# Kernel tuning notes

Hardware: AMD Instinct MI355X
Metric: run time of the kernel (lower is better)

## Reference

```python
import jax, jax.numpy as jnp
import numpy as np

N = 100000   # nodes
E = 1600000  # edges
G = 64       # graphs
D = 64       # latent_dim
NF = 128     # num_node_feats
EF = 32      # num_edge_feats
NV = 5000    # num_node_val_feats
LV = 3       # max_lv
EPS = 1e-5


def setup_inputs() -> dict:
    key = jax.random.key(0)
    ks = jax.random.split(key, 16)
    s = 0.05
    return {
        "node_feat": jax.random.normal(ks[0], (N, NF), jnp.float32),
        "edge_feat": jax.random.normal(ks[1], (E, EF), jnp.float32),
        "w_n2l_W": jax.random.normal(ks[2], (NF, D), jnp.float32) * s,
        "w_n2l_b": jnp.zeros((D,), jnp.float32),
        "node_val_embedding": jax.random.normal(ks[3], (NV, D), jnp.float32) * s,
        "w_e2l_W": jax.random.normal(ks[4], (LV + 1, EF, D), jnp.float32) * s,
        "w_e2l_b": jnp.zeros((LV + 1, D), jnp.float32),
        "conv_W": jax.random.normal(ks[5], (LV, D, D), jnp.float32) * s,
        "conv_b": jnp.zeros((LV, D), jnp.float32),
        "l2_W": jax.random.normal(ks[6], (LV, D, D), jnp.float32) * s,
        "l2_b": jnp.zeros((LV, D), jnp.float32),
        "msg_g": jnp.ones((LV + 1, D), jnp.float32),
        "msg_b": jnp.zeros((LV + 1, D), jnp.float32),
        "hid_g": jnp.ones((LV, D), jnp.float32),
        "hid_b": jnp.zeros((LV, D), jnp.float32),
        "out_W": jax.random.normal(ks[7], (D, D), jnp.float32) * s,
        "out_b": jnp.zeros((D,), jnp.float32),
        "edge_from": jax.random.randint(ks[8], (E,), 0, N, jnp.int32),
        "edge_to": jax.random.randint(ks[9], (E,), 0, N, jnp.int32),
        "g_idx": jnp.sort(jax.random.randint(ks[10], (N,), 0, G, jnp.int32)),
        "node_val_idx": jax.random.randint(ks[11], (N,), 0, NV, jnp.int32),
    }


def _bn(x, g, b):
    # BatchNorm1d in training mode: biased batch stats
    m = jnp.mean(x, axis=0)
    v = jnp.mean(jnp.square(x - m), axis=0)
    return (x - m) * jax.lax.rsqrt(v + EPS) * g + b


def reference(node_feat, edge_feat, w_n2l_W, w_n2l_b, node_val_embedding,
              w_e2l_W, w_e2l_b, conv_W, conv_b, l2_W, l2_b,
              msg_g, msg_b, hid_g, hid_b, out_W, out_b,
              edge_from, edge_to, g_idx, node_val_idx):
    act = jax.nn.relu
    # input node transform + sparse node-value embedding (one-hot spmm == gather)
    h = node_feat @ w_n2l_W + w_n2l_b + node_val_embedding[node_val_idx]
    # edge->node pool for level 0
    e0 = edge_feat @ w_e2l_W[0] + w_e2l_b[0]
    h = h + jax.ops.segment_sum(e0, edge_to, num_segments=N)
    h = _bn(act(h), msg_g[0], msg_b[0])
    for lv in range(LV):
        # MessagePassing with add-aggr: gather sources, scatter-add to targets, then Linear
        agg = jax.ops.segment_sum(h[edge_from], edge_to, num_segments=N)
        node_linear = agg @ conv_W[lv] + conv_b[lv]
        e = edge_feat @ w_e2l_W[lv + 1] + w_e2l_b[lv + 1]
        merged = act(node_linear + jax.ops.segment_sum(e, edge_to, num_segments=N))
        merged = _bn(merged, hid_g[lv], hid_b[lv])
        h = _bn(act(merged @ l2_W[lv] + l2_b[lv] + h), msg_g[lv + 1], msg_b[lv + 1])
    # readout: gnn_out='last', readout_agg='max', act_last=True, bn=False
    pooled = jax.ops.segment_max(h, g_idx, num_segments=G)
    return act(pooled @ out_W + out_b)
```

## Files before the change

kernel.cpp:

```cpp
#include <hip/hip_runtime.h>
#include <math.h>

#define NN 100000
#define EE 1600000
#define GG 64
#define DD 64
#define NF 128
#define EF 32
#define LVL 3
#define EPSBN 1e-5f
#define NTILES ((NN + 63) / 64)
#define NBKT 391

typedef unsigned short u16;
typedef unsigned int u32;
typedef short s4v __attribute__((ext_vector_type(4)));
typedef short bf16x8 __attribute__((ext_vector_type(8)));
typedef float f32x4 __attribute__((ext_vector_type(4)));

__device__ __forceinline__ float4 ld4(const float* p) { return *(const float4*)p; }
__device__ __forceinline__ u16 f2b(float f) {
    u32 u = __float_as_uint(f);
    return (u16)((u + 0x7FFFu + ((u >> 16) & 1u)) >> 16);
}
__device__ __forceinline__ float b2f(u16 u) { return __uint_as_float(((u32)u) << 16); }
__device__ __forceinline__ float blo(u32 u) { return __uint_as_float(u << 16); }
__device__ __forceinline__ float bhi(u32 u) { return __uint_as_float(u & 0xFFFF0000u); }


__global__ void k1b(const int* __restrict__ to, int* __restrict__ bhist) {
    __shared__ int h[NBKT];
    for (int i = threadIdx.x; i < NBKT; i += 256) h[i] = 0;
    __syncthreads();
    for (int e = blockIdx.x * 256 + threadIdx.x; e < EE; e += 256 * gridDim.x)
        atomicAdd(&h[to[e] >> 8], 1);
    __syncthreads();
    for (int i = threadIdx.x; i < NBKT; i += 256)
        if (h[i]) atomicAdd(&bhist[i], h[i]);
}

__global__ void k1c(const int* __restrict__ bhist, int* __restrict__ bbase,
                    int* __restrict__ gcur) {
    __shared__ int s[512];
    int t = threadIdx.x;
    s[t] = (t < NBKT) ? bhist[t] : 0;
    __syncthreads();
    for (int off = 1; off < 512; off <<= 1) {
        int v = (t >= off) ? s[t - off] : 0;
        __syncthreads();
        s[t] += v;
        __syncthreads();
    }
    if (t < NBKT) {
        int base = t ? s[t - 1] : 0;
        bbase[t] = base;
        gcur[t] = base;
    }
    if (t == NBKT - 1) bbase[NBKT] = s[t];
}

__global__ void k1d(const int* __restrict__ to, const int* __restrict__ from,
                    int* __restrict__ gcur, int2* __restrict__ tmp) {
    __shared__ int h[NBKT];
    __shared__ int cur[NBKT];
    for (int i = threadIdx.x; i < NBKT; i += 256) h[i] = 0;
    __syncthreads();
    for (int e = blockIdx.x * 256 + threadIdx.x; e < EE; e += 256 * gridDim.x)
        atomicAdd(&h[to[e] >> 8], 1);
    __syncthreads();
    for (int i = threadIdx.x; i < NBKT; i += 256)
        cur[i] = h[i] ? atomicAdd(&gcur[i], h[i]) : 0;
    __syncthreads();
    for (int e = blockIdx.x * 256 + threadIdx.x; e < EE; e += 256 * gridDim.x) {
        int tt = to[e];
        int b = tt >> 8;
        int pos = atomicAdd(&cur[b], 1);
        tmp[pos] = make_int2(from[e] | ((tt & 255) << 17), e);
    }
}

__global__ void kp2(const int2* __restrict__ tmp, const int* __restrict__ bbase,
                    int* __restrict__ row_ptr, int2* __restrict__ pair) {
    __shared__ int s[256];
    __shared__ int cur[256];
    int b = blockIdx.x, t = threadIdx.x;
    int e0 = bbase[b], e1 = bbase[b + 1];
    s[t] = 0;
    __syncthreads();
    for (int e = e0 + t; e < e1; e += 256) atomicAdd(&s[(tmp[e].x >> 17) & 255], 1);
    __syncthreads();
    int v = s[t];
    for (int off = 1; off < 256; off <<= 1) {
        int u = (t >= off) ? s[t - off] : 0;
        __syncthreads();
        s[t] += u;
        __syncthreads();
    }
    int excl = e0 + s[t] - v;
    cur[t] = excl;
    int n = b * 256 + t;
    if (n < NN) row_ptr[n] = excl;
    if (b == NBKT - 1 && t == 0) row_ptr[NN] = e1;
    __syncthreads();
    for (int e = e0 + t; e < e1; e += 256) {
        int2 w = tmp[e];
        int pos = atomicAdd(&cur[(w.x >> 17) & 255], 1);
        pair[pos] = make_int2(w.y, w.x & 0x1FFFF);
    }
}

__global__ void kpool(const float* __restrict__ ef, const int* __restrict__ row_ptr,
                      const int2* __restrict__ pair, u16* __restrict__ pooled) {
    int lane = threadIdx.x & 63;
    int wid = threadIdx.x >> 6;
    int w = lane & 31, half = lane >> 5;
    for (int n = blockIdx.x * 4 + wid; n < NN; n += gridDim.x * 4) {
        int e0 = row_ptr[n], e1 = row_ptr[n + 1];
        float acc = 0.f;
        int e = e0 + half;
        for (; e + 6 < e1; e += 8) {
            int i0 = pair[e].x, i1 = pair[e + 2].x;
            int i2 = pair[e + 4].x, i3 = pair[e + 6].x;
            float v0 = ef[(size_t)i0 * EF + w];
            float v1 = ef[(size_t)i1 * EF + w];
            float v2 = ef[(size_t)i2 * EF + w];
            float v3 = ef[(size_t)i3 * EF + w];
            acc += (v0 + v1) + (v2 + v3);
        }
        for (; e < e1; e += 2) acc += ef[(size_t)pair[e].x * EF + w];
        acc += __shfl_xor(acc, 32);
        if (half == 0) pooled[(size_t)n * EF + w] = f2b(acc);
    }
}

template <int K1, int K2, bool A1BF, bool AAFF, bool EMB, bool BE, bool RESID>
__global__ __launch_bounds__(256) void kgemm_mfma(
    const void* __restrict__ A1v, const u16* __restrict__ A2,
    const float* __restrict__ W1, const float* __restrict__ W2,
    const float* __restrict__ bias, const float* __restrict__ be,
    const int* __restrict__ row_ptr, const float* __restrict__ emb,
    const int* __restrict__ nvi, const u16* __restrict__ resid,
    const float* __restrict__ raff, const float* __restrict__ aaff,
    u16* __restrict__ Xb, float* __restrict__ stats) {
    constexpr int K = K1 + K2;
    constexpr int KP = K + 8;
    __shared__ u16 A_lds[64 * KP];
    __shared__ u16 Wt_lds[64 * KP];
    __shared__ float red[128];

    const int t = threadIdx.x;
    const int lane = t & 63;
    const int wv = t >> 6;
    const int l15 = lane & 15;
    const int lg = lane >> 4;

    for (int idx = t; idx < K * 16; idx += 256) {
        int k = idx >> 4, c4 = (idx & 15) * 4;
        float4 w4 = (k < K1) ? ld4(W1 + (size_t)k * 64 + c4)
                             : ld4(W2 + (size_t)(k - K1) * 64 + c4);
        Wt_lds[(c4 + 0) * KP + k] = f2b(w4.x);
        Wt_lds[(c4 + 1) * KP + k] = f2b(w4.y);
        Wt_lds[(c4 + 2) * KP + k] = f2b(w4.z);
        Wt_lds[(c4 + 3) * KP + k] = f2b(w4.w);
    }
    if (t < 128) red[t] = 0.f;

    float bias_c[4], be_c[4], rsc_c[4], rsh_c[4];
#pragma unroll
    for (int n = 0; n < 4; n++) {
        int ch = 16 * n + l15;
        bias_c[n] = bias[ch];
        be_c[n] = BE ? be[ch] : 0.f;
        rsc_c[n] = RESID ? raff[ch] : 0.f;
        rsh_c[n] = RESID ? raff[64 + ch] : 0.f;
    }

    for (int tile = blockIdx.x; tile < NTILES; tile += gridDim.x) {
        int nb = tile * 64;
        __syncthreads();
        if (A1BF) {
            const u16* A1b = (const u16*)A1v;
            for (int idx = t; idx < 64 * (K1 / 4); idx += 256) {
                int node = idx / (K1 / 4), kq = (idx % (K1 / 4)) * 4;
                int gn = nb + node;
                s4v v = {0, 0, 0, 0};
                if (gn < NN) {
                    v = *(const s4v*)(A1b + (size_t)gn * K1 + kq);
                    if (AAFF) {
#pragma unroll
                        for (int i = 0; i < 4; i++) {
                            float f = b2f((u16)v[i]) * aaff[kq + i] + aaff[64 + kq + i];
                            v[i] = (short)f2b(f);
                        }
                    }
                }
                *(s4v*)&A_lds[node * KP + kq] = v;
            }
        } else {
            const float* A1f = (const float*)A1v;
            for (int idx = t; idx < 64 * (K1 / 4); idx += 256) {
                int node = idx / (K1 / 4), kq = (idx % (K1 / 4)) * 4;
                int gn = nb + node;
                s4v v = {0, 0, 0, 0};
                if (gn < NN) {
                    float4 a = ld4(A1f + (size_t)gn * K1 + kq);
                    v[0] = (short)f2b(a.x); v[1] = (short)f2b(a.y);
                    v[2] = (short)f2b(a.z); v[3] = (short)f2b(a.w);
                }
                *(s4v*)&A_lds[node * KP + kq] = v;
            }
        }
        if (K2 > 0) {
            for (int idx = t; idx < 64 * (K2 / 4); idx += 256) {
                int node = idx / (K2 / 4), kq = (idx % (K2 / 4)) * 4;
                int gn = nb + node;
                s4v v = {0, 0, 0, 0};
                if (gn < NN) v = *(const s4v*)(A2 + (size_t)gn * K2 + kq);
                *(s4v*)&A_lds[node * KP + K1 + kq] = v;
            }
        }
        __syncthreads();

        f32x4 acc[4];
#pragma unroll
        for (int n = 0; n < 4; n++) acc[n] = (f32x4){0.f, 0.f, 0.f, 0.f};
        const int arow = 16 * wv + l15;
#pragma unroll
        for (int kk = 0; kk < K; kk += 32) {
            s4v alo = *(const s4v*)&A_lds[arow * KP + kk + lg * 4];
            s4v ahi = *(const s4v*)&A_lds[arow * KP + kk + lg * 4 + 16];
            bf16x8 a = __builtin_shufflevector(alo, ahi, 0, 1, 2, 3, 4, 5, 6, 7);
#pragma unroll
            for (int n = 0; n < 4; n++) {
                s4v wlo = *(const s4v*)&Wt_lds[(16 * n + l15) * KP + kk + lg * 4];
                s4v whi = *(const s4v*)&Wt_lds[(16 * n + l15) * KP + kk + lg * 4 + 16];
                bf16x8 b = __builtin_shufflevector(wlo, whi, 0, 1, 2, 3, 4, 5, 6, 7);
                acc[n] = __builtin_amdgcn_mfma_f32_16x16x32_bf16(a, b, acc[n], 0, 0, 0);
            }
        }

        float ss[4] = {0, 0, 0, 0}, sq2[4] = {0, 0, 0, 0};
#pragma unroll
        for (int r = 0; r < 4; r++) {
            int node = nb + 16 * wv + lg * 4 + r;
            if (node < NN) {
                float deg = BE ? (float)(row_ptr[node + 1] - row_ptr[node]) : 0.f;
                int nv = EMB ? nvi[node] : 0;
#pragma unroll
                for (int n = 0; n < 4; n++) {
                    int ch = 16 * n + l15;
                    float v = acc[n][r] + bias_c[n];
                    if (BE) v += deg * be_c[n];
                    if (EMB) v += emb[(size_t)nv * 64 + ch];
                    if (RESID) v += b2f(resid[(size_t)node * 64 + ch]) * rsc_c[n] + rsh_c[n];
                    v = fmaxf(v, 0.f);
                    Xb[(size_t)node * 64 + ch] = f2b(v);
                    ss[n] += v;
                    sq2[n] += v * v;
                }
            }
        }
#pragma unroll
        for (int n = 0; n < 4; n++) {
            float a = ss[n];
            a += __shfl_xor(a, 16);
            a += __shfl_xor(a, 32);
            float b = sq2[n];
            b += __shfl_xor(b, 16);
            b += __shfl_xor(b, 32);
            if (lg == 0) {
                atomicAdd(&red[16 * n + l15], a);
                atomicAdd(&red[64 + 16 * n + l15], b);
            }
        }
    }
    __syncthreads();
    if (t < 128) atomicAdd(&stats[t], red[t]);
}

__global__ void kfin(float* __restrict__ stats, const float* __restrict__ g,
                     const float* __restrict__ b, int slot) {
    int t = threadIdx.x;
    float mean = stats[t] * (1.0f / NN);
    float var = stats[64 + t] * (1.0f / NN) - mean * mean;
    float rstd = rsqrtf(fmaxf(var, 0.f) + EPSBN);
    float sc = g[t] * rstd;
    float* slotp = stats + 128 + slot * 128;
    slotp[t] = sc;
    slotp[64 + t] = b[t] - mean * sc;
    stats[t] = 0.f;
    stats[64 + t] = 0.f;
}

__global__ void kmsg_bf(const u32* __restrict__ h2, const int* __restrict__ row_ptr,
                        const int2* __restrict__ pair, const float* __restrict__ aff,
                        u32* __restrict__ agg) {
    int lane = threadIdx.x & 63;
    int wid = threadIdx.x >> 6;
    int w = lane & 31, half = lane >> 5;
    float sc0 = aff[2 * w], sc1 = aff[2 * w + 1];
    float sh0 = aff[64 + 2 * w], sh1 = aff[64 + 2 * w + 1];
    for (int n = blockIdx.x * 4 + wid; n < NN; n += gridDim.x * 4) {
        int e0 = row_ptr[n], e1 = row_ptr[n + 1];
        float a0 = 0.f, a1 = 0.f;
        int e = e0;
        for (; e + 16 <= e1; e += 16) {
            int s0 = pair[e + half].y, s1 = pair[e + 2 + half].y;
            int s2 = pair[e + 4 + half].y, s3 = pair[e + 6 + half].y;
            int s4 = pair[e + 8 + half].y, s5 = pair[e + 10 + half].y;
            int s6 = pair[e + 12 + half].y, s7 = pair[e + 14 + half].y;
            u32 u0 = h2[(size_t)s0 * 32 + w];
            u32 u1 = h2[(size_t)s1 * 32 + w];
            u32 u2 = h2[(size_t)s2 * 32 + w];
            u32 u3 = h2[(size_t)s3 * 32 + w];
            u32 u4 = h2[(size_t)s4 * 32 + w];
            u32 u5 = h2[(size_t)s5 * 32 + w];
            u32 u6 = h2[(size_t)s6 * 32 + w];
            u32 u7 = h2[(size_t)s7 * 32 + w];
            a0 += ((blo(u0) + blo(u1)) + (blo(u2) + blo(u3))) +
                  ((blo(u4) + blo(u5)) + (blo(u6) + blo(u7)));
            a1 += ((bhi(u0) + bhi(u1)) + (bhi(u2) + bhi(u3))) +
                  ((bhi(u4) + bhi(u5)) + (bhi(u6) + bhi(u7)));
        }
        for (; e + 8 <= e1; e += 8) {
            int s0 = pair[e + half].y, s1 = pair[e + 2 + half].y;
            int s2 = pair[e + 4 + half].y, s3 = pair[e + 6 + half].y;
            u32 u0 = h2[(size_t)s0 * 32 + w];
            u32 u1 = h2[(size_t)s1 * 32 + w];
            u32 u2 = h2[(size_t)s2 * 32 + w];
            u32 u3 = h2[(size_t)s3 * 32 + w];
            a0 += (blo(u0) + blo(u1)) + (blo(u2) + blo(u3));
            a1 += (bhi(u0) + bhi(u1)) + (bhi(u2) + bhi(u3));
        }
        for (; e < e1; e += 2) {
            if (e + half < e1) {
                u32 u = h2[(size_t)pair[e + half].y * 32 + w];
                a0 += blo(u);
                a1 += bhi(u);
            }
        }
        a0 += __shfl_xor(a0, 32);
        a1 += __shfl_xor(a1, 32);
        if (half == 0) {
            float deg = (float)(e1 - e0);
            u16 o0 = f2b(sc0 * a0 + deg * sh0);
            u16 o1 = f2b(sc1 * a1 + deg * sh1);
            agg[(size_t)n * 32 + w] = (u32)o0 | ((u32)o1 << 16);
        }
    }
}

__device__ __forceinline__ unsigned fenc(float f) {
    unsigned u = __float_as_uint(f);
    return (u >> 31) ? ~u : (u | 0x80000000u);
}
__device__ __forceinline__ float fdec(unsigned k) {
    return (k >> 31) ? __uint_as_float(k ^ 0x80000000u) : __uint_as_float(~k);
}

__global__ void kinitpk(unsigned* __restrict__ pk) {
    int i = blockIdx.x * blockDim.x + threadIdx.x;
    if (i < GG * DD) pk[i] = 0x007FFFFFu;
}

__global__ void kread(const u16* __restrict__ h2, const int* __restrict__ gidx,
                      const float* __restrict__ aff, unsigned* __restrict__ pk) {
    int lane = threadIdx.x & 63;
    int wid = threadIdx.x >> 6;
    float sc = aff[lane], sh = aff[64 + lane];
    int gw = blockIdx.x * 4 + wid;
    int nw = gridDim.x * 4;
    int chunk = (NN + nw - 1) / nw;
    int lo = gw * chunk, hi = min(lo + chunk, NN);
    if (lo >= hi) return;
    int cur = gidx[lo];
    float acc = -INFINITY;
    for (int n = lo; n < hi; n++) {
        int g = gidx[n];
        if (g != cur) {
            atomicMax(&pk[cur * DD + lane], fenc(acc));
            cur = g;
            acc = -INFINITY;
        }
        acc = fmaxf(acc, b2f(h2[(size_t)n * 64 + lane]) * sc + sh);
    }
    atomicMax(&pk[cur * DD + lane], fenc(acc));
}

__global__ void kout(const unsigned* __restrict__ pk, const float* __restrict__ W,
                     const float* __restrict__ b, float* __restrict__ out) {
    int t = blockIdx.x * blockDim.x + threadIdx.x;
    int g = t >> 6, d = t & 63;
    float acc = b[d];
    for (int k = 0; k < DD; k++) {
        float p = fdec(pk[g * DD + k]);
        acc += p * W[k * DD + d];
    }
    out[t] = fmaxf(acc, 0.f);
}

extern "C" void kernel_launch(void* const* d_in, const int* in_sizes, int n_in,
                              void* d_out, int out_size, void* d_ws, size_t ws_size,
                              hipStream_t stream) {
    const float* node_feat = (const float*)d_in[0];
    const float* edge_feat = (const float*)d_in[1];
    const float* w_n2l_W = (const float*)d_in[2];
    const float* w_n2l_b = (const float*)d_in[3];
    const float* nve = (const float*)d_in[4];
    const float* w_e2l_W = (const float*)d_in[5];
    const float* w_e2l_b = (const float*)d_in[6];
    const float* conv_W = (const float*)d_in[7];
    const float* conv_b = (const float*)d_in[8];
    const float* l2_W = (const float*)d_in[9];
    const float* l2_b = (const float*)d_in[10];
    const float* msg_g = (const float*)d_in[11];
    const float* msg_b = (const float*)d_in[12];
    const float* hid_g = (const float*)d_in[13];
    const float* hid_b = (const float*)d_in[14];
    const float* out_W = (const float*)d_in[15];
    const float* out_b = (const float*)d_in[16];
    const int* edge_from = (const int*)d_in[17];
    const int* edge_to = (const int*)d_in[18];
    const int* g_idx = (const int*)d_in[19];
    const int* nvi = (const int*)d_in[20];
    float* out = (float*)d_out;

    char* ws = (char*)d_ws;
    size_t off = 0;
    auto alloc = [&](size_t bytes) -> void* {
        void* p = ws + off;
        off += (bytes + 255) / 256 * 256;
        return p;
    };
    int* row_ptr = (int*)alloc((size_t)(NN + 1) * 4);
    int2* pair = (int2*)alloc((size_t)EE * 8);
    int2* tmp = (int2*)alloc((size_t)EE * 8);
    u16* pooled_ef = (u16*)alloc((size_t)NN * EF * 2);
    u16* h2a = (u16*)alloc((size_t)NN * DD * 2);
    u16* h2b = (u16*)alloc((size_t)NN * DD * 2);
    u16* agg_bf = (u16*)alloc((size_t)NN * DD * 2);
    u16* mb_bf = (u16*)alloc((size_t)NN * DD * 2);
    float* stats = (float*)alloc(1024 * 4);
    unsigned* pk = (unsigned*)alloc((size_t)GG * DD * 4);
    int* bhist = (int*)alloc((size_t)NBKT * 4);
    int* bbase = (int*)alloc((size_t)(NBKT + 1) * 4);
    int* gcur = (int*)alloc((size_t)NBKT * 4);
    (void)ws_size; (void)n_in; (void)in_sizes; (void)out_size;

    hipMemsetAsync(bhist, 0, (size_t)NBKT * 4, stream);
    hipMemsetAsync(stats, 0, 1024 * 4, stream);
    kinitpk<<<16, 256, 0, stream>>>(pk);

    k1b<<<256, 256, 0, stream>>>(edge_to, bhist);
    k1c<<<1, 512, 0, stream>>>(bhist, bbase, gcur);
    k1d<<<256, 256, 0, stream>>>(edge_to, edge_from, gcur, tmp);
    kp2<<<NBKT, 256, 0, stream>>>(tmp, bbase, row_ptr, pair);
    kpool<<<2048, 256, 0, stream>>>(edge_feat, row_ptr, pair, pooled_ef);

    const int GB = 782;

    kgemm_mfma<NF, EF, false, false, true, true, false>
        <<<GB, 256, 0, stream>>>(node_feat, pooled_ef, w_n2l_W, w_e2l_W,
                                 w_n2l_b, w_e2l_b, row_ptr, nve, nvi,
                                 nullptr, nullptr, nullptr, h2a, stats);
    kfin<<<1, 64, 0, stream>>>(stats, msg_g, msg_b, 0);

    u16* hcur = h2a;
    u16* hnext = h2b;
    for (int lv = 0; lv < LVL; lv++) {
        kmsg_bf<<<2048, 256, 0, stream>>>((const u32*)hcur, row_ptr, pair,
                                          stats + 128 + lv * 128, (u32*)agg_bf);
        kgemm_mfma<DD, EF, true, false, false, true, false>
            <<<GB, 256, 0, stream>>>(agg_bf, pooled_ef, conv_W + lv * DD * DD,
                                     w_e2l_W + (size_t)(lv + 1) * EF * DD,
                                     conv_b + lv * DD,
                                     w_e2l_b + (size_t)(lv + 1) * DD, row_ptr,
                                     nullptr, nullptr, nullptr, nullptr, nullptr,
                                     mb_bf, stats);
        kfin<<<1, 64, 0, stream>>>(stats, hid_g + lv * DD, hid_b + lv * DD, 4 + lv);
        kgemm_mfma<DD, 0, true, true, false, false, true>
            <<<GB, 256, 0, stream>>>(mb_bf, nullptr, l2_W + lv * DD * DD, nullptr,
                                     l2_b + lv * DD, nullptr, row_ptr, nullptr,
                                     nullptr, hcur, stats + 128 + lv * 128,
                                     stats + 128 + (4 + lv) * 128, hnext, stats);
        kfin<<<1, 64, 0, stream>>>(stats, msg_g + (lv + 1) * DD, msg_b + (lv + 1) * DD,
                                   lv + 1);
        u16* tmp2 = hcur; hcur = hnext; hnext = tmp2;
    }

    kread<<<1024, 256, 0, stream>>>(hcur, g_idx, stats + 128 + LVL * 128, pk);
    kout<<<GG, 64, 0, stream>>>(pk, out_W, out_b, out);
}
```

Before: 584.5 us.

## Fuse message gather into merge GEMM and split edge pairs into SoA arrays

The per-level gather-and-sum of neighbour features now happens inside the merge GEMM kernel. Each block aggregates its 64-node tile straight into LDS, then runs the MFMA GEMM, so the bf16 agg buffer is no longer written to and re-read from global memory and one launch per level disappears. The int2 pair array is also split into separate source and edge-id arrays, so each gather reads only the index it needs. The cost is less gather parallelism: 782 blocks with each wave walking 16 nodes in sequence, instead of 2048 blocks in a grid-stride loop, which can reduce latency hiding for the irregular loads.

```diff
diff --git a/kernel.cpp b/kernel.cpp
--- a/kernel.cpp
+++ b/kernel.cpp
@@ -27,7 +27,6 @@
 __device__ __forceinline__ float blo(u32 u) { return __uint_as_float(u << 16); }
 __device__ __forceinline__ float bhi(u32 u) { return __uint_as_float(u & 0xFFFF0000u); }
 
-
 __global__ void k1b(const int* __restrict__ to, int* __restrict__ bhist) {
     __shared__ int h[NBKT];
     for (int i = threadIdx.x; i < NBKT; i += 256) h[i] = 0;
@@ -80,7 +79,8 @@
 }
 
 __global__ void kp2(const int2* __restrict__ tmp, const int* __restrict__ bbase,
-                    int* __restrict__ row_ptr, int2* __restrict__ pair) {
+                    int* __restrict__ row_ptr, int* __restrict__ src_s,
+                    int* __restrict__ eid_s) {
     __shared__ int s[256];
     __shared__ int cur[256];
     int b = blockIdx.x, t = threadIdx.x;
@@ -105,12 +105,13 @@
     for (int e = e0 + t; e < e1; e += 256) {
         int2 w = tmp[e];
         int pos = atomicAdd(&cur[(w.x >> 17) & 255], 1);
-        pair[pos] = make_int2(w.y, w.x & 0x1FFFF);
+        src_s[pos] = w.x & 0x1FFFF;
+        eid_s[pos] = w.y;
     }
 }
 
 __global__ void kpool(const float* __restrict__ ef, const int* __restrict__ row_ptr,
-                      const int2* __restrict__ pair, u16* __restrict__ pooled) {
+                      const int* __restrict__ eid_s, u16* __restrict__ pooled) {
     int lane = threadIdx.x & 63;
     int wid = threadIdx.x >> 6;
     int w = lane & 31, half = lane >> 5;
@@ -119,15 +120,15 @@
         float acc = 0.f;
         int e = e0 + half;
         for (; e + 6 < e1; e += 8) {
-            int i0 = pair[e].x, i1 = pair[e + 2].x;
-            int i2 = pair[e + 4].x, i3 = pair[e + 6].x;
+            int i0 = eid_s[e], i1 = eid_s[e + 2];
+            int i2 = eid_s[e + 4], i3 = eid_s[e + 6];
             float v0 = ef[(size_t)i0 * EF + w];
             float v1 = ef[(size_t)i1 * EF + w];
             float v2 = ef[(size_t)i2 * EF + w];
             float v3 = ef[(size_t)i3 * EF + w];
             acc += (v0 + v1) + (v2 + v3);
         }
-        for (; e < e1; e += 2) acc += ef[(size_t)pair[e].x * EF + w];
+        for (; e < e1; e += 2) acc += ef[(size_t)eid_s[e] * EF + w];
         acc += __shfl_xor(acc, 32);
         if (half == 0) pooled[(size_t)n * EF + w] = f2b(acc);
     }
@@ -278,6 +279,164 @@
     if (t < 128) atomicAdd(&stats[t], red[t]);
 }
 
+__global__ __launch_bounds__(256) void kmerge_fused(
+    const u32* __restrict__ h2, const int* __restrict__ row_ptr,
+    const int* __restrict__ src_s, const u16* __restrict__ pooled,
+    const float* __restrict__ cW, const float* __restrict__ We,
+    const float* __restrict__ cb, const float* __restrict__ be,
+    const float* __restrict__ aff, u16* __restrict__ Xb,
+    float* __restrict__ stats) {
+    constexpr int K = DD + EF;
+    constexpr int KP = K + 8;
+    __shared__ u16 A_lds[64 * KP];
+    __shared__ u16 Wt_lds[64 * KP];
+    __shared__ float red[128];
+
+    const int t = threadIdx.x;
+    const int lane = t & 63;
+    const int wv = t >> 6;
+    const int l15 = lane & 15;
+    const int lg = lane >> 4;
+    const int w = lane & 31, half = lane >> 5;
+
+    for (int idx = t; idx < K * 16; idx += 256) {
+        int k = idx >> 4, c4 = (idx & 15) * 4;
+        float4 w4 = (k < DD) ? ld4(cW + (size_t)k * 64 + c4)
+                             : ld4(We + (size_t)(k - DD) * 64 + c4);
+        Wt_lds[(c4 + 0) * KP + k] = f2b(w4.x);
+        Wt_lds[(c4 + 1) * KP + k] = f2b(w4.y);
+        Wt_lds[(c4 + 2) * KP + k] = f2b(w4.z);
+        Wt_lds[(c4 + 3) * KP + k] = f2b(w4.w);
+    }
+    if (t < 128) red[t] = 0.f;
+
+    float sc0 = aff[2 * w], sc1 = aff[2 * w + 1];
+    float sh0 = aff[64 + 2 * w], sh1 = aff[64 + 2 * w + 1];
+
+    float bias_c[4], be_c[4];
+#pragma unroll
+    for (int n = 0; n < 4; n++) {
+        int ch = 16 * n + l15;
+        bias_c[n] = cb[ch];
+        be_c[n] = be[ch];
+    }
+
+    for (int tile = blockIdx.x; tile < NTILES; tile += gridDim.x) {
+        int nb = tile * 64;
+        __syncthreads();
+        for (int idx = t; idx < 64 * 8; idx += 256) {
+            int node = idx >> 3, kq = (idx & 7) * 4;
+            int gn = nb + node;
+            s4v v = {0, 0, 0, 0};
+            if (gn < NN) v = *(const s4v*)(pooled + (size_t)gn * EF + kq);
+            *(s4v*)&A_lds[node * KP + DD + kq] = v;
+        }
+        for (int ii = 0; ii < 16; ii++) {
+            int nloc = 16 * wv + ii;
+            int gn = nb + nloc;
+            int e0 = 0, e1 = 0;
+            if (gn < NN) { e0 = row_ptr[gn]; e1 = row_ptr[gn + 1]; }
+            float a0 = 0.f, a1 = 0.f;
+            int e = e0;
+            for (; e + 16 <= e1; e += 16) {
+                int s0 = src_s[e + half], s1 = src_s[e + 2 + half];
+                int s2 = src_s[e + 4 + half], s3 = src_s[e + 6 + half];
+                int s4 = src_s[e + 8 + half], s5 = src_s[e + 10 + half];
+                int s6 = src_s[e + 12 + half], s7 = src_s[e + 14 + half];
+                u32 u0 = h2[(size_t)s0 * 32 + w];
+                u32 u1 = h2[(size_t)s1 * 32 + w];
+                u32 u2 = h2[(size_t)s2 * 32 + w];
+                u32 u3 = h2[(size_t)s3 * 32 + w];
+                u32 u4 = h2[(size_t)s4 * 32 + w];
+                u32 u5 = h2[(size_t)s5 * 32 + w];
+                u32 u6 = h2[(size_t)s6 * 32 + w];
+                u32 u7 = h2[(size_t)s7 * 32 + w];
+                a0 += ((blo(u0) + blo(u1)) + (blo(u2) + blo(u3))) +
+                      ((blo(u4) + blo(u5)) + (blo(u6) + blo(u7)));
+                a1 += ((bhi(u0) + bhi(u1)) + (bhi(u2) + bhi(u3))) +
+                      ((bhi(u4) + bhi(u5)) + (bhi(u6) + bhi(u7)));
+            }
+            for (; e + 8 <= e1; e += 8) {
+                int s0 = src_s[e + half], s1 = src_s[e + 2 + half];
+                int s2 = src_s[e + 4 + half], s3 = src_s[e + 6 + half];
+                u32 u0 = h2[(size_t)s0 * 32 + w];
+                u32 u1 = h2[(size_t)s1 * 32 + w];
+                u32 u2 = h2[(size_t)s2 * 32 + w];
+                u32 u3 = h2[(size_t)s3 * 32 + w];
+                a0 += (blo(u0) + blo(u1)) + (blo(u2) + blo(u3));
+                a1 += (bhi(u0) + bhi(u1)) + (bhi(u2) + bhi(u3));
+            }
+            for (; e < e1; e += 2) {
+                if (e + half < e1) {
+                    u32 u = h2[(size_t)src_s[e + half] * 32 + w];
+                    a0 += blo(u);
+                    a1 += bhi(u);
+                }
+            }
+            a0 += __shfl_xor(a0, 32);
+            a1 += __shfl_xor(a1, 32);
+            if (half == 0) {
+                float deg = (float)(e1 - e0);
+                u16 o0 = f2b(sc0 * a0 + deg * sh0);
+                u16 o1 = f2b(sc1 * a1 + deg * sh1);
+                *(u32*)&A_lds[nloc * KP + 2 * w] = (u32)o0 | ((u32)o1 << 16);
+            }
+        }
+        __syncthreads();
+
+        f32x4 acc[4];
+#pragma unroll
+        for (int n = 0; n < 4; n++) acc[n] = (f32x4){0.f, 0.f, 0.f, 0.f};
+        const int arow = 16 * wv + l15;
+#pragma unroll
+        for (int kk = 0; kk < K; kk += 32) {
+            s4v alo = *(const s4v*)&A_lds[arow * KP + kk + lg * 4];
+            s4v ahi = *(const s4v*)&A_lds[arow * KP + kk + lg * 4 + 16];
+            bf16x8 a = __builtin_shufflevector(alo, ahi, 0, 1, 2, 3, 4, 5, 6, 7);
+#pragma unroll
+            for (int n = 0; n < 4; n++) {
+                s4v wlo = *(const s4v*)&Wt_lds[(16 * n + l15) * KP + kk + lg * 4];
+                s4v whi = *(const s4v*)&Wt_lds[(16 * n + l15) * KP + kk + lg * 4 + 16];
+                bf16x8 b = __builtin_shufflevector(wlo, whi, 0, 1, 2, 3, 4, 5, 6, 7);
+                acc[n] = __builtin_amdgcn_mfma_f32_16x16x32_bf16(a, b, acc[n], 0, 0, 0);
+            }
+        }
+
+        float ss[4] = {0, 0, 0, 0}, sq2[4] = {0, 0, 0, 0};
+#pragma unroll
+        for (int r = 0; r < 4; r++) {
+            int node = nb + 16 * wv + lg * 4 + r;
+            if (node < NN) {
+                float deg = (float)(row_ptr[node + 1] - row_ptr[node]);
+#pragma unroll
+                for (int n = 0; n < 4; n++) {
+                    int ch = 16 * n + l15;
+                    float v = acc[n][r] + bias_c[n] + deg * be_c[n];
+                    v = fmaxf(v, 0.f);
+                    Xb[(size_t)node * 64 + ch] = f2b(v);
+                    ss[n] += v;
+                    sq2[n] += v * v;
+                }
+            }
+        }
+#pragma unroll
+        for (int n = 0; n < 4; n++) {
+            float a = ss[n];
+            a += __shfl_xor(a, 16);
+            a += __shfl_xor(a, 32);
+            float b = sq2[n];
+            b += __shfl_xor(b, 16);
+            b += __shfl_xor(b, 32);
+            if (lg == 0) {
+                atomicAdd(&red[16 * n + l15], a);
+                atomicAdd(&red[64 + 16 * n + l15], b);
+            }
+        }
+    }
+    __syncthreads();
+    if (t < 128) atomicAdd(&stats[t], red[t]);
+}
+
 __global__ void kfin(float* __restrict__ stats, const float* __restrict__ g,
                      const float* __restrict__ b, int slot) {
     int t = threadIdx.x;
@@ -290,64 +449,6 @@
     slotp[64 + t] = b[t] - mean * sc;
     stats[t] = 0.f;
     stats[64 + t] = 0.f;
-}
-
-__global__ void kmsg_bf(const u32* __restrict__ h2, const int* __restrict__ row_ptr,
-                        const int2* __restrict__ pair, const float* __restrict__ aff,
-                        u32* __restrict__ agg) {
-    int lane = threadIdx.x & 63;
-    int wid = threadIdx.x >> 6;
-    int w = lane & 31, half = lane >> 5;
-    float sc0 = aff[2 * w], sc1 = aff[2 * w + 1];
-    float sh0 = aff[64 + 2 * w], sh1 = aff[64 + 2 * w + 1];
-    for (int n = blockIdx.x * 4 + wid; n < NN; n += gridDim.x * 4) {
-        int e0 = row_ptr[n], e1 = row_ptr[n + 1];
-        float a0 = 0.f, a1 = 0.f;
-        int e = e0;
-        for (; e + 16 <= e1; e += 16) {
-            int s0 = pair[e + half].y, s1 = pair[e + 2 + half].y;
-            int s2 = pair[e + 4 + half].y, s3 = pair[e + 6 + half].y;
-            int s4 = pair[e + 8 + half].y, s5 = pair[e + 10 + half].y;
-            int s6 = pair[e + 12 + half].y, s7 = pair[e + 14 + half].y;
-            u32 u0 = h2[(size_t)s0 * 32 + w];
-            u32 u1 = h2[(size_t)s1 * 32 + w];
-            u32 u2 = h2[(size_t)s2 * 32 + w];
-            u32 u3 = h2[(size_t)s3 * 32 + w];
-            u32 u4 = h2[(size_t)s4 * 32 + w];
-            u32 u5 = h2[(size_t)s5 * 32 + w];
-            u32 u6 = h2[(size_t)s6 * 32 + w];
-            u32 u7 = h2[(size_t)s7 * 32 + w];
-            a0 += ((blo(u0) + blo(u1)) + (blo(u2) + blo(u3))) +
-                  ((blo(u4) + blo(u5)) + (blo(u6) + blo(u7)));
-            a1 += ((bhi(u0) + bhi(u1)) + (bhi(u2) + bhi(u3))) +
-                  ((bhi(u4) + bhi(u5)) + (bhi(u6) + bhi(u7)));
-        }
-        for (; e + 8 <= e1; e += 8) {
-            int s0 = pair[e + half].y, s1 = pair[e + 2 + half].y;
-            int s2 = pair[e + 4 + half].y, s3 = pair[e + 6 + half].y;
-            u32 u0 = h2[(size_t)s0 * 32 + w];
-            u32 u1 = h2[(size_t)s1 * 32 + w];
-            u32 u2 = h2[(size_t)s2 * 32 + w];
-            u32 u3 = h2[(size_t)s3 * 32 + w];
-            a0 += (blo(u0) + blo(u1)) + (blo(u2) + blo(u3));
-            a1 += (bhi(u0) + bhi(u1)) + (bhi(u2) + bhi(u3));
-        }
-        for (; e < e1; e += 2) {
-            if (e + half < e1) {
-                u32 u = h2[(size_t)pair[e + half].y * 32 + w];
-                a0 += blo(u);
-                a1 += bhi(u);
-            }
-        }
-        a0 += __shfl_xor(a0, 32);
-        a1 += __shfl_xor(a1, 32);
-        if (half == 0) {
-            float deg = (float)(e1 - e0);
-            u16 o0 = f2b(sc0 * a0 + deg * sh0);
-            u16 o1 = f2b(sc1 * a1 + deg * sh1);
-            agg[(size_t)n * 32 + w] = (u32)o0 | ((u32)o1 << 16);
-        }
-    }
 }
 
 __device__ __forceinline__ unsigned fenc(float f) {
@@ -433,12 +534,12 @@
         return p;
     };
     int* row_ptr = (int*)alloc((size_t)(NN + 1) * 4);
-    int2* pair = (int2*)alloc((size_t)EE * 8);
+    int* src_s = (int*)alloc((size_t)EE * 4);
+    int* eid_s = (int*)alloc((size_t)EE * 4);
     int2* tmp = (int2*)alloc((size_t)EE * 8);
     u16* pooled_ef = (u16*)alloc((size_t)NN * EF * 2);
     u16* h2a = (u16*)alloc((size_t)NN * DD * 2);
     u16* h2b = (u16*)alloc((size_t)NN * DD * 2);
-    u16* agg_bf = (u16*)alloc((size_t)NN * DD * 2);
     u16* mb_bf = (u16*)alloc((size_t)NN * DD * 2);
     float* stats = (float*)alloc(1024 * 4);
     unsigned* pk = (unsigned*)alloc((size_t)GG * DD * 4);
@@ -454,8 +555,8 @@
     k1b<<<256, 256, 0, stream>>>(edge_to, bhist);
     k1c<<<1, 512, 0, stream>>>(bhist, bbase, gcur);
     k1d<<<256, 256, 0, stream>>>(edge_to, edge_from, gcur, tmp);
-    kp2<<<NBKT, 256, 0, stream>>>(tmp, bbase, row_ptr, pair);
-    kpool<<<2048, 256, 0, stream>>>(edge_feat, row_ptr, pair, pooled_ef);
+    kp2<<<NBKT, 256, 0, stream>>>(tmp, bbase, row_ptr, src_s, eid_s);
+    kpool<<<2048, 256, 0, stream>>>(edge_feat, row_ptr, eid_s, pooled_ef);
 
     const int GB = 782;
 
@@ -468,15 +569,10 @@
     u16* hcur = h2a;
     u16* hnext = h2b;
     for (int lv = 0; lv < LVL; lv++) {
-        kmsg_bf<<<2048, 256, 0, stream>>>((const u32*)hcur, row_ptr, pair,
-                                          stats + 128 + lv * 128, (u32*)agg_bf);
-        kgemm_mfma<DD, EF, true, false, false, true, false>
-            <<<GB, 256, 0, stream>>>(agg_bf, pooled_ef, conv_W + lv * DD * DD,
-                                     w_e2l_W + (size_t)(lv + 1) * EF * DD,
-                                     conv_b + lv * DD,
-                                     w_e2l_b + (size_t)(lv + 1) * DD, row_ptr,
-                                     nullptr, nullptr, nullptr, nullptr, nullptr,
-                                     mb_bf, stats);
+        kmerge_fused<<<GB, 256, 0, stream>>>(
+            (const u32*)hcur, row_ptr, src_s, pooled_ef, conv_W + lv * DD * DD,
+            w_e2l_W + (size_t)(lv + 1) * EF * DD, conv_b + lv * DD,
+            w_e2l_b + (size_t)(lv + 1) * DD, stats + 128 + lv * 128, mb_bf, stats);
         kfin<<<1, 64, 0, stream>>>(stats, hid_g + lv * DD, hid_b + lv * DD, 4 + lv);
         kgemm_mfma<DD, 0, true, true, false, false, true>
             <<<GB, 256, 0, stream>>>(mb_bf, nullptr, l2_W + lv * DD * DD, nullptr,
```

Result: slower. 673.1 us (+15.2%).

## Split edge pair array into SoA and widen gather loads to 4 edge slots

Applied to the files above, without the earlier changes.

The interleaved (edge id, source) pair array becomes two separate int arrays, so the pooling and message kernels each read only the index stream they need. Both gather kernels now use 16 lanes per row with wider per-lane loads (float2 for edge features, 64-bit for bf16 node rows), processing 4 edges per wave step instead of 2. Grid sizes are doubled. This is meant to cut index bandwidth and raise memory-level parallelism in the irregular gathers, at the cost of an extra shuffle reduction step and more partial work per row.

```diff
diff --git a/kernel.cpp b/kernel.cpp
--- a/kernel.cpp
+++ b/kernel.cpp
@@ -14,6 +14,7 @@
 
 typedef unsigned short u16;
 typedef unsigned int u32;
+typedef unsigned long long u64;
 typedef short s4v __attribute__((ext_vector_type(4)));
 typedef short bf16x8 __attribute__((ext_vector_type(8)));
 typedef float f32x4 __attribute__((ext_vector_type(4)));
@@ -26,7 +27,6 @@
 __device__ __forceinline__ float b2f(u16 u) { return __uint_as_float(((u32)u) << 16); }
 __device__ __forceinline__ float blo(u32 u) { return __uint_as_float(u << 16); }
 __device__ __forceinline__ float bhi(u32 u) { return __uint_as_float(u & 0xFFFF0000u); }
-
 
 __global__ void k1b(const int* __restrict__ to, int* __restrict__ bhist) {
     __shared__ int h[NBKT];
@@ -80,7 +80,8 @@
 }
 
 __global__ void kp2(const int2* __restrict__ tmp, const int* __restrict__ bbase,
-                    int* __restrict__ row_ptr, int2* __restrict__ pair) {
+                    int* __restrict__ row_ptr, int* __restrict__ src_s,
+                    int* __restrict__ eid_s) {
     __shared__ int s[256];
     __shared__ int cur[256];
     int b = blockIdx.x, t = threadIdx.x;
@@ -105,31 +106,42 @@
     for (int e = e0 + t; e < e1; e += 256) {
         int2 w = tmp[e];
         int pos = atomicAdd(&cur[(w.x >> 17) & 255], 1);
-        pair[pos] = make_int2(w.y, w.x & 0x1FFFF);
+        src_s[pos] = w.x & 0x1FFFF;
+        eid_s[pos] = w.y;
     }
 }
 
 __global__ void kpool(const float* __restrict__ ef, const int* __restrict__ row_ptr,
-                      const int2* __restrict__ pair, u16* __restrict__ pooled) {
+                      const int* __restrict__ eid_s, u16* __restrict__ pooled) {
     int lane = threadIdx.x & 63;
     int wid = threadIdx.x >> 6;
-    int w = lane & 31, half = lane >> 5;
+    int w = lane & 15, slot = lane >> 4;
     for (int n = blockIdx.x * 4 + wid; n < NN; n += gridDim.x * 4) {
         int e0 = row_ptr[n], e1 = row_ptr[n + 1];
-        float acc = 0.f;
-        int e = e0 + half;
-        for (; e + 6 < e1; e += 8) {
-            int i0 = pair[e].x, i1 = pair[e + 2].x;
-            int i2 = pair[e + 4].x, i3 = pair[e + 6].x;
-            float v0 = ef[(size_t)i0 * EF + w];
-            float v1 = ef[(size_t)i1 * EF + w];
-            float v2 = ef[(size_t)i2 * EF + w];
-            float v3 = ef[(size_t)i3 * EF + w];
-            acc += (v0 + v1) + (v2 + v3);
-        }
-        for (; e < e1; e += 2) acc += ef[(size_t)pair[e].x * EF + w];
-        acc += __shfl_xor(acc, 32);
-        if (half == 0) pooled[(size_t)n * EF + w] = f2b(acc);
+        float ax = 0.f, ay = 0.f;
+        int e = e0 + slot;
+        for (; e + 12 < e1; e += 16) {
+            int i0 = eid_s[e], i1 = eid_s[e + 4], i2 = eid_s[e + 8], i3 = eid_s[e + 12];
+            float2 v0 = *(const float2*)(ef + (size_t)i0 * EF + 2 * w);
+            float2 v1 = *(const float2*)(ef + (size_t)i1 * EF + 2 * w);
+            float2 v2 = *(const float2*)(ef + (size_t)i2 * EF + 2 * w);
+            float2 v3 = *(const float2*)(ef + (size_t)i3 * EF + 2 * w);
+            ax += (v0.x + v1.x) + (v2.x + v3.x);
+            ay += (v0.y + v1.y) + (v2.y + v3.y);
+        }
+        for (; e < e1; e += 4) {
+            float2 v = *(const float2*)(ef + (size_t)eid_s[e] * EF + 2 * w);
+            ax += v.x;
+            ay += v.y;
+        }
+        ax += __shfl_xor(ax, 16);
+        ax += __shfl_xor(ax, 32);
+        ay += __shfl_xor(ay, 16);
+        ay += __shfl_xor(ay, 32);
+        if (slot == 0) {
+            u32 o = (u32)f2b(ax) | ((u32)f2b(ay) << 16);
+            *(u32*)&pooled[(size_t)n * EF + 2 * w] = o;
+        }
     }
 }
 
@@ -292,60 +304,56 @@
     stats[64 + t] = 0.f;
 }
 
-__global__ void kmsg_bf(const u32* __restrict__ h2, const int* __restrict__ row_ptr,
-                        const int2* __restrict__ pair, const float* __restrict__ aff,
-                        u32* __restrict__ agg) {
+__global__ void kmsg_bf(const u64* __restrict__ h4, const int* __restrict__ row_ptr,
+                        const int* __restrict__ src_s, const float* __restrict__ aff,
+                        u64* __restrict__ agg) {
     int lane = threadIdx.x & 63;
     int wid = threadIdx.x >> 6;
-    int w = lane & 31, half = lane >> 5;
-    float sc0 = aff[2 * w], sc1 = aff[2 * w + 1];
-    float sh0 = aff[64 + 2 * w], sh1 = aff[64 + 2 * w + 1];
+    int w = lane & 15, slot = lane >> 4;
+    float sc0 = aff[4 * w], sc1 = aff[4 * w + 1];
+    float sc2 = aff[4 * w + 2], sc3 = aff[4 * w + 3];
+    float sh0 = aff[64 + 4 * w], sh1 = aff[64 + 4 * w + 1];
+    float sh2 = aff[64 + 4 * w + 2], sh3 = aff[64 + 4 * w + 3];
     for (int n = blockIdx.x * 4 + wid; n < NN; n += gridDim.x * 4) {
         int e0 = row_ptr[n], e1 = row_ptr[n + 1];
-        float a0 = 0.f, a1 = 0.f;
-        int e = e0;
-        for (; e + 16 <= e1; e += 16) {
-            int s0 = pair[e + half].y, s1 = pair[e + 2 + half].y;
-            int s2 = pair[e + 4 + half].y, s3 = pair[e + 6 + half].y;
-            int s4 = pair[e + 8 + half].y, s5 = pair[e + 10 + half].y;
-            int s6 = pair[e + 12 + half].y, s7 = pair[e + 14 + half].y;
-            u32 u0 = h2[(size_t)s0 * 32 + w];
-            u32 u1 = h2[(size_t)s1 * 32 + w];
-            u32 u2 = h2[(size_t)s2 * 32 + w];
-            u32 u3 = h2[(size_t)s3 * 32 + w];
-            u32 u4 = h2[(size_t)s4 * 32 + w];
-            u32 u5 = h2[(size_t)s5 * 32 + w];
-            u32 u6 = h2[(size_t)s6 * 32 + w];
-            u32 u7 = h2[(size_t)s7 * 32 + w];
-            a0 += ((blo(u0) + blo(u1)) + (blo(u2) + blo(u3))) +
-                  ((blo(u4) + blo(u5)) + (blo(u6) + blo(u7)));
-            a1 += ((bhi(u0) + bhi(u1)) + (bhi(u2) + bhi(u3))) +
-                  ((bhi(u4) + bhi(u5)) + (bhi(u6) + bhi(u7)));
-        }
-        for (; e + 8 <= e1; e += 8) {
-            int s0 = pair[e + half].y, s1 = pair[e + 2 + half].y;
-            int s2 = pair[e + 4 + half].y, s3 = pair[e + 6 + half].y;
-            u32 u0 = h2[(size_t)s0 * 32 + w];
-            u32 u1 = h2[(size_t)s1 * 32 + w];
-            u32 u2 = h2[(size_t)s2 * 32 + w];
-            u32 u3 = h2[(size_t)s3 * 32 + w];
-            a0 += (blo(u0) + blo(u1)) + (blo(u2) + blo(u3));
-            a1 += (bhi(u0) + bhi(u1)) + (bhi(u2) + bhi(u3));
-        }
-        for (; e < e1; e += 2) {
-            if (e + half < e1) {
-                u32 u = h2[(size_t)pair[e + half].y * 32 + w];
-                a0 += blo(u);
-                a1 += bhi(u);
-            }
-        }
+        float a0 = 0.f, a1 = 0.f, a2 = 0.f, a3 = 0.f;
+        int e = e0 + slot;
+        for (; e + 12 < e1; e += 16) {
+            int s0 = src_s[e], s1 = src_s[e + 4], s2 = src_s[e + 8], s3 = src_s[e + 12];
+            u64 v0 = h4[(size_t)s0 * 16 + w];
+            u64 v1 = h4[(size_t)s1 * 16 + w];
+            u64 v2 = h4[(size_t)s2 * 16 + w];
+            u64 v3 = h4[(size_t)s3 * 16 + w];
+            u32 l0 = (u32)v0, h0 = (u32)(v0 >> 32);
+            u32 l1 = (u32)v1, h1 = (u32)(v1 >> 32);
+            u32 l2 = (u32)v2, h2w = (u32)(v2 >> 32);
+            u32 l3 = (u32)v3, h3 = (u32)(v3 >> 32);
+            a0 += (blo(l0) + blo(l1)) + (blo(l2) + blo(l3));
+            a1 += (bhi(l0) + bhi(l1)) + (bhi(l2) + bhi(l3));
+            a2 += (blo(h0) + blo(h1)) + (blo(h2w) + blo(h3));
+            a3 += (bhi(h0) + bhi(h1)) + (bhi(h2w) + bhi(h3));
+        }
+        for (; e < e1; e += 4) {
+            u64 v = h4[(size_t)src_s[e] * 16 + w];
+            u32 l = (u32)v, h = (u32)(v >> 32);
+            a0 += blo(l);
+            a1 += bhi(l);
+            a2 += blo(h);
+            a3 += bhi(h);
+        }
+        a0 += __shfl_xor(a0, 16);
         a0 += __shfl_xor(a0, 32);
+        a1 += __shfl_xor(a1, 16);
         a1 += __shfl_xor(a1, 32);
-        if (half == 0) {
+        a2 += __shfl_xor(a2, 16);
+        a2 += __shfl_xor(a2, 32);
+        a3 += __shfl_xor(a3, 16);
+        a3 += __shfl_xor(a3, 32);
+        if (slot == 0) {
             float deg = (float)(e1 - e0);
-            u16 o0 = f2b(sc0 * a0 + deg * sh0);
-            u16 o1 = f2b(sc1 * a1 + deg * sh1);
-            agg[(size_t)n * 32 + w] = (u32)o0 | ((u32)o1 << 16);
+            u32 lo = (u32)f2b(sc0 * a0 + deg * sh0) | ((u32)f2b(sc1 * a1 + deg * sh1) << 16);
+            u32 hi = (u32)f2b(sc2 * a2 + deg * sh2) | ((u32)f2b(sc3 * a3 + deg * sh3) << 16);
+            agg[(size_t)n * 16 + w] = (u64)lo | ((u64)hi << 32);
         }
     }
 }
@@ -433,7 +441,8 @@
         return p;
     };
     int* row_ptr = (int*)alloc((size_t)(NN + 1) * 4);
-    int2* pair = (int2*)alloc((size_t)EE * 8);
+    int* src_s = (int*)alloc((size_t)EE * 4);
+    int* eid_s = (int*)alloc((size_t)EE * 4);
     int2* tmp = (int2*)alloc((size_t)EE * 8);
     u16* pooled_ef = (u16*)alloc((size_t)NN * EF * 2);
     u16* h2a = (u16*)alloc((size_t)NN * DD * 2);
@@ -454,8 +463,8 @@
     k1b<<<256, 256, 0, stream>>>(edge_to, bhist);
     k1c<<<1, 512, 0, stream>>>(bhist, bbase, gcur);
     k1d<<<256, 256, 0, stream>>>(edge_to, edge_from, gcur, tmp);
-    kp2<<<NBKT, 256, 0, stream>>>(tmp, bbase, row_ptr, pair);
-    kpool<<<2048, 256, 0, stream>>>(edge_feat, row_ptr, pair, pooled_ef);
+    kp2<<<NBKT, 256, 0, stream>>>(tmp, bbase, row_ptr, src_s, eid_s);
+    kpool<<<4096, 256, 0, stream>>>(edge_feat, row_ptr, eid_s, pooled_ef);
 
     const int GB = 782;
 
@@ -468,8 +477,8 @@
     u16* hcur = h2a;
     u16* hnext = h2b;
     for (int lv = 0; lv < LVL; lv++) {
-        kmsg_bf<<<2048, 256, 0, stream>>>((const u32*)hcur, row_ptr, pair,
-                                          stats + 128 + lv * 128, (u32*)agg_bf);
+        kmsg_bf<<<4096, 256, 0, stream>>>((const u64*)hcur, row_ptr, src_s,
+                                          stats + 128 + lv * 128, (u64*)agg_bf);
         kgemm_mfma<DD, EF, true, false, false, true, false>
             <<<GB, 256, 0, stream>>>(agg_bf, pooled_ef, conv_W + lv * DD * DD,
                                      w_e2l_W + (size_t)(lv + 1) * EF * DD,
```

Result: no change. 586.3 us (+0.3%).
